# Kernel optimization log

Measured on AMD Instinct MI355X. Metric: run time of the kernel, lower is better.

Reference implementation:

```python
import jax, jax.numpy as jnp
import numpy as np
from jax import lax

B, T, D_IN = 16, 512, 128
H_ENC, D_LAT, H_CTX, H_PRED = 512, 256, 512, 512
K_STEPS, TEMP = 12, 0.1


def setup_inputs() -> dict:
    ks = jax.random.split(jax.random.key(0), 8)
    def w(i, fi, fo):
        return jax.random.normal(ks[i], (fi, fo), jnp.float32) * (1.0 / float(np.sqrt(fi)))
    return {
        "x": jax.random.normal(ks[0], (B, T, D_IN), jnp.float32),
        "enc_w1": w(1, D_IN, H_ENC), "enc_b1": jnp.zeros((H_ENC,), jnp.float32),
        "enc_w2": w(2, H_ENC, H_ENC), "enc_b2": jnp.zeros((H_ENC,), jnp.float32),
        "enc_w3": w(3, H_ENC, D_LAT), "enc_b3": jnp.zeros((D_LAT,), jnp.float32),
        "gru_wi": w(4, D_LAT, 3 * H_CTX), "gru_bi": jnp.zeros((3 * H_CTX,), jnp.float32),
        "gru_wh": w(5, H_CTX, 3 * H_CTX), "gru_bhn": jnp.zeros((H_CTX,), jnp.float32),
        "pred_w1": w(6, H_CTX, H_PRED), "pred_b1": jnp.zeros((H_PRED,), jnp.float32),
        "pred_w2": w(7, H_PRED, D_LAT), "pred_b2": jnp.zeros((D_LAT,), jnp.float32),
    }


def _gru(z, gru_wi, gru_bi, gru_wh, gru_bhn):
    # flax GRUCell: r=sig(Wir x + bir + Whr h); u=sig(Wiz x + biz + Whz h);
    Bsz = z.shape[0]
    H = gru_wh.shape[0]
    xi = z @ gru_wi + gru_bi          # [B, T, 3H] precomputed input projections
    xi = jnp.swapaxes(xi, 0, 1)       # [T, B, 3H]

    def step(h, x_t):
        hp = h @ gru_wh               # [B, 3H]
        xr, xu, xn = jnp.split(x_t, 3, axis=-1)
        hr, hu, hn = jnp.split(hp, 3, axis=-1)
        r = jax.nn.sigmoid(xr + hr)
        u = jax.nn.sigmoid(xu + hu)
        n = jnp.tanh(xn + r * (hn + gru_bhn))
        h_new = (1.0 - u) * n + u * h
        return h_new, h_new

    h0 = jnp.zeros((Bsz, H), z.dtype)
    _, outs = lax.scan(step, h0, xi)  # [T, B, H]
    return jnp.swapaxes(outs, 0, 1)   # [B, T, H]


def reference(x, enc_w1, enc_b1, enc_w2, enc_b2, enc_w3, enc_b3,
              gru_wi, gru_bi, gru_wh, gru_bhn,
              pred_w1, pred_b1, pred_w2, pred_b2):
    # Encoder MLP
    h = jax.nn.relu(x @ enc_w1 + enc_b1)
    h = jax.nn.relu(h @ enc_w2 + enc_b2)
    z = h @ enc_w3 + enc_b3                         # [B, T, D_LAT]
    # GRU context network
    c = _gru(z, gru_wi, gru_bi, gru_wh, gru_bhn)    # [B, T, H_CTX]
    # InfoNCE loss (prediction net is identical across k, so hoist it)
    c_t = c[:, :-K_STEPS, :].reshape(-1, c.shape[-1])   # [N, H_CTX], N=B*(T-K)
    p = jax.nn.relu(c_t @ pred_w1 + pred_b1) @ pred_w2 + pred_b2
    p = p / jnp.linalg.norm(p, axis=1, keepdims=True)   # [N, D_LAT]
    total = jnp.zeros((), z.dtype)
    for k in range(1, K_STEPS + 1):
        zt = z[:, k:T - K_STEPS + k, :].reshape(-1, z.shape[-1])
        zt = zt / jnp.linalg.norm(zt, axis=1, keepdims=True)
        sim = (p @ zt.T) / TEMP                         # [N, N]
        # -mean(diag(log_softmax)) = -mean(diag(sim) - logsumexp(sim, axis=1))
        total = total + (-jnp.mean(jnp.diagonal(sim) - jax.nn.logsumexp(sim, axis=1)))
    loss = total / K_STEPS
    return z, c, loss
```

## Files before the change

### kernel.cpp

```cpp
#include <hip/hip_runtime.h>
#include <cstdint>
#include <cstddef>

typedef unsigned short u16;
typedef unsigned int   u32;
typedef unsigned long long u64;
typedef __attribute__((ext_vector_type(8))) short bf16x8;
typedef __attribute__((ext_vector_type(4))) float f32x4;
typedef __attribute__((ext_vector_type(4))) unsigned int u32x4;

typedef __attribute__((address_space(1))) const unsigned int as1c_uint;
typedef __attribute__((address_space(3))) unsigned int as3_uint;

__device__ __forceinline__ void async16(const void* g, void* l) {
  __builtin_amdgcn_global_load_lds((as1c_uint*)g, (as3_uint*)l, 16, 0, 0);
}
__device__ __forceinline__ float bf2f(u16 u) {
  return __uint_as_float(((u32)u) << 16);
}
__device__ __forceinline__ u16 f2bf(float x) {
  u32 u = __float_as_uint(x);
  u32 r = u + 0x7FFFu + ((u >> 16) & 1u);
  return (u16)(r >> 16);
}

__device__ __forceinline__ u32 ld_u32_ic(const void* p) {
  u32 v;
  asm volatile("global_load_dword %0, %1, off sc0 sc1\n\ts_waitcnt vmcnt(0)"
               : "=v"(v) : "v"(p) : "memory");
  return v;
}
__device__ __forceinline__ void st_u32_ic(void* p, u32 v) {
  asm volatile("global_store_dword %0, %1, off sc0 sc1" :: "v"(p), "v"(v) : "memory");
}
__device__ __forceinline__ void ld_h64_ic(const void* p, u32x4& a, u32x4& b,
                                          u32x4& c, u32x4& d) {
  asm volatile(
      "global_load_dwordx4 %0, %4, off sc0 sc1\n\t"
      "global_load_dwordx4 %1, %4, off offset:16 sc0 sc1\n\t"
      "global_load_dwordx4 %2, %4, off offset:32 sc0 sc1\n\t"
      "global_load_dwordx4 %3, %4, off offset:48 sc0 sc1\n\t"
      "s_waitcnt vmcnt(0)"
      : "=&v"(a), "=&v"(b), "=&v"(c), "=&v"(d) : "v"(p) : "memory");
}

__global__ void cvt_k(const float4* __restrict__ in, ushort4* __restrict__ out) {
  int i = blockIdx.x * 256 + threadIdx.x;
  float4 v = in[i];
  ushort4 o;
  o.x = f2bf(v.x); o.y = f2bf(v.y); o.z = f2bf(v.z); o.w = f2bf(v.w);
  out[i] = o;
}

__global__ void tr_k(const float* __restrict__ in, u16* __restrict__ out, int K, int N) {
  __shared__ u16 t[32][33];
  int bn = blockIdx.x * 32, bk = blockIdx.y * 32;
  int x = threadIdx.x, y = threadIdx.y;
#pragma unroll
  for (int i = 0; i < 32; i += 8)
    t[y + i][x] = f2bf(in[(size_t)(bk + y + i) * N + bn + x]);
  __syncthreads();
#pragma unroll
  for (int i = 0; i < 32; i += 8)
    out[(size_t)(bn + y + i) * K + bk + x] = t[x][y + i];
}

__global__ __launch_bounds__(256) void gemm_k(
    const u16* __restrict__ A, const u16* __restrict__ Bt,
    const float* __restrict__ bias, u16* __restrict__ Cbf, float* __restrict__ Cf,
    int N, int K, int act) {
  __shared__ __align__(16) u16 As[128 * 32];
  __shared__ __align__(16) u16 Bs[128 * 32];
  int tid = threadIdx.x;
  int lane = tid & 63, w = tid >> 6;
  int wm = w >> 1, wn = w & 1;
  int mm = lane & 15, kh = lane >> 4;
  int m0 = blockIdx.y * 128, n0 = blockIdx.x * 128;

  f32x4 zero = {0.f, 0.f, 0.f, 0.f};
  f32x4 acc[4][4];
#pragma unroll
  for (int i = 0; i < 4; ++i)
#pragma unroll
    for (int j = 0; j < 4; ++j) acc[i][j] = zero;

  for (int kt = 0; kt < K; kt += 32) {
#pragma unroll
    for (int it = 0; it < 2; ++it) {
      int q = tid + it * 256;
      int row = q >> 2, kc = (q & 3) * 8;
      async16(A  + (size_t)(m0 + row) * K + kt + kc, &As[q * 8]);
      async16(Bt + (size_t)(n0 + row) * K + kt + kc, &Bs[q * 8]);
    }
    __syncthreads();
    bf16x8 av[4], bv[4];
#pragma unroll
    for (int i = 0; i < 4; ++i) {
      av[i] = *(const bf16x8*)&As[(wm * 64 + i * 16 + mm) * 32 + kh * 8];
      bv[i] = *(const bf16x8*)&Bs[(wn * 64 + i * 16 + mm) * 32 + kh * 8];
    }
#pragma unroll
    for (int im = 0; im < 4; ++im)
#pragma unroll
      for (int in = 0; in < 4; ++in)
        acc[im][in] = __builtin_amdgcn_mfma_f32_16x16x32_bf16(av[im], bv[in], acc[im][in], 0, 0, 0);
    __syncthreads();
  }

#pragma unroll
  for (int im = 0; im < 4; ++im)
#pragma unroll
    for (int in = 0; in < 4; ++in)
#pragma unroll
      for (int r = 0; r < 4; ++r) {
        int gm = m0 + wm * 64 + im * 16 + kh * 4 + r;
        int gn = n0 + wn * 64 + in * 16 + mm;
        float v = acc[im][in][r] + bias[gn];
        if (act) v = fmaxf(v, 0.f);
        size_t off = (size_t)gm * N + gn;
        if (Cbf) Cbf[off] = f2bf(v);
        if (Cf)  Cf[off]  = v;
      }
}

__global__ __launch_bounds__(256) void norm_k(const u16* __restrict__ in,
                                              u16* __restrict__ out, int pack) {
  int row = blockIdx.x * 4 + (threadIdx.x >> 6);
  int lane = threadIdx.x & 63;
  ushort4 v = ((const ushort4*)(in + (size_t)row * 256))[lane];
  float a = bf2f(v.x), b = bf2f(v.y), c = bf2f(v.z), d = bf2f(v.w);
  float s = a * a + b * b + c * c + d * d;
#pragma unroll
  for (int o = 32; o; o >>= 1) s += __shfl_xor(s, o);
  float rn = rsqrtf(s);
  int orow = row;
  if (pack) {
    int bb = row >> 9, tt = row & 511;
    if (tt >= 500) return;
    orow = bb * 500 + tt;
  }
  ushort4 o4;
  o4.x = f2bf(a * rn); o4.y = f2bf(b * rn);
  o4.z = f2bf(c * rn); o4.w = f2bf(d * rn);
  *(ushort4*)(out + (size_t)orow * 256 + lane * 4) = o4;
}

#define HS 520

__global__ __launch_bounds__(512, 1) void gru_k(
    const u16* __restrict__ xi, const float* __restrict__ WH,
    const float* __restrict__ BHN, float* __restrict__ cf,
    u16* __restrict__ cbf, u16* hbuf, u32* flags) {
  __shared__ __align__(16) u16 hs[16 * HS];
  __shared__ float xis[2 * 1536];
  __shared__ float gts[1536];
  __shared__ float hnf[512];

  int tid = threadIdx.x;
  int role = blockIdx.x;
  int c0 = role * 32;

  int lane = tid & 63, w = tid >> 6;
  int mm = lane & 15, kh = lane >> 4;

  bf16x8 wf[16];
  if (w < 6) {
    int gcol = (w >> 1) * 512 + c0 + (w & 1) * 16 + mm;
    int kb = kh * 8;
#pragma unroll
    for (int kk = 0; kk < 16; ++kk) {
      bf16x8 tf;
#pragma unroll
      for (int j = 0; j < 8; ++j)
        tf[j] = (short)f2bf(WH[(size_t)(kk * 32 + kb + j) * 1536 + gcol]);
      wf[kk] = tf;
    }
  }
  int cr = tid >> 4, cj = (tid & 15) * 2;
  float bhn0 = 0.f, bhn1 = 0.f;
  if (w < 4) { bhn0 = BHN[c0 + cj]; bhn1 = BHN[c0 + cj + 1]; }

  int tt = tid - 384;
  size_t xoff[12];
  u16 xpre[12];
  if (w >= 6) {
#pragma unroll
    for (int j = 0; j < 12; ++j) {
      int v = j * 128 + tt;
      int b = v / 96, q = v - b * 96;
      int gcol = (q >> 5) * 512 + c0 + (q & 31);
      xoff[j] = (size_t)b * 512 * 1536 + gcol;
      xis[v] = bf2f(xi[xoff[j]]);
    }
#pragma unroll
    for (int j = 0; j < 12; ++j) xpre[j] = xi[xoff[j] + 1536];
  }

  for (int t = 0; t < 512; ++t) {
    if (w < 4) {
      if (t == 0) {
        for (int i = tid; i < 16 * HS; i += 256) hs[i] = 0;
      } else {
        int iter = 0;
        const u32* fl = &flags[tid & 15];
        while (ld_u32_ic(fl) < (u32)t) { if (++iter > (1 << 22)) break; }
        const u16* hb = hbuf + (size_t)(t & 1) * 8192 + (tid >> 4) * 512 + (tid & 15) * 32;
        u32x4 a, b, c, d;
        ld_h64_ic(hb, a, b, c, d);
        u32x4* dst = (u32x4*)&hs[(tid >> 4) * HS + (tid & 15) * 32];
        dst[0] = a; dst[1] = b; dst[2] = c; dst[3] = d;
      }
    } else if (w >= 6) {
      if (t > 0) {
        int v = tt * 4;
        int b = v >> 5, col = v & 31;
        size_t co = ((size_t)b * 512 + (t - 1)) * 512 + c0 + col;
        float4 o;
        o.x = hnf[v]; o.y = hnf[v + 1]; o.z = hnf[v + 2]; o.w = hnf[v + 3];
        *(float4*)&cf[co] = o;
        uint2 pk;
        pk.x = (u32)f2bf(o.x) | ((u32)f2bf(o.y) << 16);
        pk.y = (u32)f2bf(o.z) | ((u32)f2bf(o.w) << 16);
        *(uint2*)&cbf[co] = pk;
      }
      if (t < 511) {
        float* xd = &xis[((t + 1) & 1) * 1536];
#pragma unroll
        for (int j = 0; j < 12; ++j) xd[j * 128 + tt] = bf2f(xpre[j]);
      }
      if (t < 510) {
        const u16* xs = xi + (size_t)(t + 2) * 1536;
#pragma unroll
        for (int j = 0; j < 12; ++j) xpre[j] = xs[xoff[j]];
      }
    }
    __syncthreads();

    if (w < 6) {
      f32x4 acc = {0.f, 0.f, 0.f, 0.f};
#pragma unroll
      for (int kk = 0; kk < 16; ++kk) {
        bf16x8 a = *(const bf16x8*)&hs[mm * HS + kk * 32 + kh * 8];
        acc = __builtin_amdgcn_mfma_f32_16x16x32_bf16(a, wf[kk], acc, 0, 0, 0);
      }
      int gc = (w >> 1) * 32 + (w & 1) * 16 + mm;
#pragma unroll
      for (int r = 0; r < 4; ++r) gts[(kh * 4 + r) * 96 + gc] = acc[r];
    }
    __syncthreads();

    if (w < 4) {
      const float* xc = &xis[(t & 1) * 1536] + cr * 96;
      const float* gr_ = &gts[cr * 96];
      float hp0 = bf2f(hs[cr * HS + c0 + cj]);
      float hp1 = bf2f(hs[cr * HS + c0 + cj + 1]);
      float r0 = 1.f / (1.f + __expf(-(xc[cj] + gr_[cj])));
      float u0 = 1.f / (1.f + __expf(-(xc[32 + cj] + gr_[32 + cj])));
      float nx0 = xc[64 + cj] + r0 * (gr_[64 + cj] + bhn0);
      float n0 = 1.f - 2.f / (__expf(2.f * nx0) + 1.f);
      float h0 = (1.f - u0) * n0 + u0 * hp0;
      float r1 = 1.f / (1.f + __expf(-(xc[cj + 1] + gr_[cj + 1])));
      float u1 = 1.f / (1.f + __expf(-(xc[33 + cj] + gr_[33 + cj])));
      float nx1 = xc[65 + cj] + r1 * (gr_[65 + cj] + bhn1);
      float n1 = 1.f - 2.f / (__expf(2.f * nx1) + 1.f);
      float h1v = (1.f - u1) * n1 + u1 * hp1;
      hnf[cr * 32 + cj] = h0;
      hnf[cr * 32 + cj + 1] = h1v;
      u32 pk = (u32)f2bf(h0) | ((u32)f2bf(h1v) << 16);
      st_u32_ic(hbuf + (size_t)((t + 1) & 1) * 8192 + cr * 512 + c0 + cj, pk);
      asm volatile("s_waitcnt vmcnt(0)" ::: "memory");
    }
    __syncthreads();
    if (tid == 0) st_u32_ic(&flags[role], (u32)(t + 1));
  }

  if (w >= 6) {
    int v = tt * 4;
    int b = v >> 5, col = v & 31;
    size_t co = ((size_t)b * 512 + 511) * 512 + c0 + col;
    float4 o;
    o.x = hnf[v]; o.y = hnf[v + 1]; o.z = hnf[v + 2]; o.w = hnf[v + 3];
    *(float4*)&cf[co] = o;
    uint2 pk;
    pk.x = (u32)f2bf(o.x) | ((u32)f2bf(o.y) << 16);
    pk.y = (u32)f2bf(o.z) | ((u32)f2bf(o.w) << 16);
    *(uint2*)&cbf[co] = pk;
  }
}

__global__ __launch_bounds__(256) void sgemm_k(
    const u16* __restrict__ P, const u16* __restrict__ Z,
    float* __restrict__ g, float* __restrict__ diag) {
  __shared__ __align__(16) u16 Ap[128 * 256];
  __shared__ __align__(16) u16 Bs[128 * 32];
  __shared__ float gacc[128 * 128];
  int tid = threadIdx.x;
  int lane = tid & 63, w = tid >> 6;
  int wm = w >> 1, wn = w & 1;
  int mm = lane & 15, kh = lane >> 4;
  int r0 = blockIdx.y * 128, t0 = blockIdx.x * 128;

#pragma unroll
  for (int it = 0; it < 16; ++it) {
    int q = tid + it * 256;
    int row = q >> 5, kc = (q & 31) * 8;
    async16(P + (size_t)(r0 + row) * 256 + kc, &Ap[q * 8]);
  }
  for (int i = tid; i < 128 * 128; i += 256) gacc[i] = 0.f;
  __syncthreads();

  f32x4 zero = {0.f, 0.f, 0.f, 0.f};
  for (int b = 0; b < 16; ++b) {
    int n0 = b * 512 + t0;
    f32x4 acc[4][4];
#pragma unroll
    for (int i = 0; i < 4; ++i)
#pragma unroll
      for (int j = 0; j < 4; ++j) acc[i][j] = zero;

    for (int kk = 0; kk < 8; ++kk) {
#pragma unroll
      for (int it = 0; it < 2; ++it) {
        int q = tid + it * 256;
        int row = q >> 2, kc = (q & 3) * 8;
        async16(Z + (size_t)(n0 + row) * 256 + kk * 32 + kc, &Bs[q * 8]);
      }
      __syncthreads();
      bf16x8 av[4], bv[4];
#pragma unroll
      for (int i = 0; i < 4; ++i) {
        av[i] = *(const bf16x8*)&Ap[(wm * 64 + i * 16 + mm) * 256 + kk * 32 + kh * 8];
        bv[i] = *(const bf16x8*)&Bs[(wn * 64 + i * 16 + mm) * 32 + kh * 8];
      }
#pragma unroll
      for (int im = 0; im < 4; ++im)
#pragma unroll
        for (int in = 0; in < 4; ++in)
          acc[im][in] = __builtin_amdgcn_mfma_f32_16x16x32_bf16(av[im], bv[in], acc[im][in], 0, 0, 0);
      __syncthreads();
    }
#pragma unroll
    for (int im = 0; im < 4; ++im)
#pragma unroll
      for (int in = 0; in < 4; ++in)
#pragma unroll
        for (int r = 0; r < 4; ++r) {
          int row = wm * 64 + im * 16 + kh * 4 + r;
          int col = wn * 64 + in * 16 + mm;
          float s10 = acc[im][in][r] * 10.f;
          gacc[row * 128 + col] += __expf(s10 - 10.f);
          int ig = r0 + row;
          if (ig < 8000) {
            int bi = ig / 500;
            if (bi == b) {
              int ti = ig - bi * 500;
              int dt = t0 + col - ti;
              if (dt >= 1 && dt <= 12) diag[(size_t)ig * 12 + dt - 1] = s10;
            }
          }
        }
  }
  __syncthreads();
  for (int i = tid; i < 128 * 128; i += 256) {
    int row = i >> 7, col = i & 127;
    g[(size_t)(r0 + row) * 512 + t0 + col] = gacc[i];
  }
}

__global__ __launch_bounds__(256) void win_k(const float* __restrict__ g,
                                             const float* __restrict__ diag,
                                             float* __restrict__ acc) {
  __shared__ float lo[4][16], hi[4][16];
  int w = threadIdx.x >> 6, lane = threadIdx.x & 63;
  int row = blockIdx.x * 4 + w;
  const float* gr = g + (size_t)row * 512;
  float4 a = ((const float4*)gr)[lane * 2];
  float4 b = ((const float4*)gr)[lane * 2 + 1];
  float s = a.x + a.y + a.z + a.w + b.x + b.y + b.z + b.w;
#pragma unroll
  for (int o = 32; o; o >>= 1) s += __shfl_xor(s, o);
  if (lane == 0) { lo[w][0]=a.x; lo[w][1]=a.y; lo[w][2]=a.z; lo[w][3]=a.w;
                   lo[w][4]=b.x; lo[w][5]=b.y; lo[w][6]=b.z; lo[w][7]=b.w; }
  if (lane == 1) { lo[w][8]=a.x; lo[w][9]=a.y; lo[w][10]=a.z; lo[w][11]=a.w; }
  if (lane == 62){ hi[w][0]=b.x; hi[w][1]=b.y; hi[w][2]=b.z; hi[w][3]=b.w; }
  if (lane == 63){ hi[w][4]=a.x; hi[w][5]=a.y; hi[w][6]=a.z; hi[w][7]=a.w;
                   hi[w][8]=b.x; hi[w][9]=b.y; hi[w][10]=b.z; hi[w][11]=b.w; }
  __syncthreads();
  float term = 0.f;
  if (lane < 12) {
    int k = lane + 1;
    float pre = 0.f, suf = 0.f;
#pragma unroll
    for (int j = 0; j < 12; ++j) {
      if (j < k) pre += lo[w][j];
      if (j >= k) suf += hi[w][j];
    }
    float W = s - pre - suf;
    term = diag[(size_t)row * 12 + lane] - __logf(W) - 10.f;
  }
#pragma unroll
  for (int o = 32; o; o >>= 1) term += __shfl_xor(term, o);
  if (lane == 0) atomicAdd(acc, term);
}

__global__ void fin_k(const float* acc, float* lout) {
  lout[0] = -acc[0] * (1.f / 96000.f);
}

extern "C" void kernel_launch(void* const* d_in, const int* in_sizes, int n_in,
                              void* d_out, int out_size, void* d_ws, size_t ws_size,
                              hipStream_t stream) {
  (void)in_sizes; (void)n_in; (void)out_size; (void)ws_size;
  const float* x    = (const float*)d_in[0];
  const float* ew1  = (const float*)d_in[1];
  const float* eb1  = (const float*)d_in[2];
  const float* ew2  = (const float*)d_in[3];
  const float* eb2  = (const float*)d_in[4];
  const float* ew3  = (const float*)d_in[5];
  const float* eb3  = (const float*)d_in[6];
  const float* gwi  = (const float*)d_in[7];
  const float* gbi  = (const float*)d_in[8];
  const float* gwh  = (const float*)d_in[9];
  const float* gbhn = (const float*)d_in[10];
  const float* pw1  = (const float*)d_in[11];
  const float* pb1  = (const float*)d_in[12];
  const float* pw2  = (const float*)d_in[13];
  const float* pb2  = (const float*)d_in[14];

  char* W = (char*)d_ws;
  u32*   flags = (u32*)(W + 64);
  float* lacc = (float*)(W + 2048);
  u16*   w1T  = (u16*)(W + 4096);
  u16*   w2T  = (u16*)(W + 135168);
  u16*   w3T  = (u16*)(W + 659456);
  u16*   wiT  = (u16*)(W + 921600);
  u16*   p1T  = (u16*)(W + 1708032);
  u16*   p2T  = (u16*)(W + 2232320);
  u16*   hbuf = (u16*)(W + 2494464);
  float* diag = (float*)(W + 2527232);
  u16*   zhat = (u16*)(W + 2911232);
  u16*   zbf  = (u16*)(W + 7105536);
  u16*   cbf  = (u16*)(W + 7105536);
  u16*   ppk  = (u16*)(W + 7105536);
  u16*   xi   = (u16*)(W + 15494144);
  u16*   xbf  = (u16*)(W + 15494144);
  u16*   h1   = (u16*)(W + 17591296);
  u16*   h2   = (u16*)(W + 25979904);
  float* g    = (float*)(W + 15494144);

  float* zf    = (float*)d_out;
  float* cf    = zf + 2097152;
  float* lout  = zf + 6291456;

  hipMemsetAsync(d_ws, 0, 4096, stream);

  cvt_k<<<1024, 256, 0, stream>>>((const float4*)x, (ushort4*)xbf);

  dim3 tb(32, 8);
  tr_k<<<dim3(16, 4),  tb, 0, stream>>>(ew1, w1T, 128, 512);
  tr_k<<<dim3(16, 16), tb, 0, stream>>>(ew2, w2T, 512, 512);
  tr_k<<<dim3(8, 16),  tb, 0, stream>>>(ew3, w3T, 512, 256);
  tr_k<<<dim3(48, 8),  tb, 0, stream>>>(gwi, wiT, 256, 1536);
  tr_k<<<dim3(16, 16), tb, 0, stream>>>(pw1, p1T, 512, 512);
  tr_k<<<dim3(8, 16),  tb, 0, stream>>>(pw2, p2T, 512, 256);

  gemm_k<<<dim3(4, 64),  256, 0, stream>>>(xbf,  w1T, eb1, h1,  nullptr, 512, 128, 1);
  gemm_k<<<dim3(4, 64),  256, 0, stream>>>(h1,   w2T, eb2, h2,  nullptr, 512, 512, 1);
  gemm_k<<<dim3(2, 64),  256, 0, stream>>>(h2,   w3T, eb3, zbf, zf,      256, 512, 0);
  norm_k<<<2048, 256, 0, stream>>>(zbf, zhat, 0);
  gemm_k<<<dim3(12, 64), 256, 0, stream>>>(zbf,  wiT, gbi, xi,  nullptr, 1536, 256, 0);
  gru_k<<<16, 512, 0, stream>>>(xi, gwh, gbhn, cf, cbf, hbuf, flags);
  gemm_k<<<dim3(4, 64),  256, 0, stream>>>(cbf,  p1T, pb1, h1,  nullptr, 512, 512, 1);
  gemm_k<<<dim3(2, 64),  256, 0, stream>>>(h1,   p2T, pb2, h2,  nullptr, 256, 512, 0);
  norm_k<<<2048, 256, 0, stream>>>(h2, ppk, 1);
  sgemm_k<<<dim3(4, 63), 256, 0, stream>>>(ppk, zhat, g, diag);
  win_k<<<2000, 256, 0, stream>>>(g, diag, lacc);
  fin_k<<<1, 1, 0, stream>>>(lacc, lout);
}
```

Measured before the change: 1.910 ms.

## Embed step tags in GRU hidden-state exchange instead of separate flag handshake

The cross-block GRU synchronisation no longer uses a per-block flag that is written after a barrier and then polled before the hidden state is read. Each 4-byte bf16 pair is now stored together with its timestep tag as an 8-byte unit, and consumers poll the data itself until every tag matches. This removes the store-wait, flag store and separate flag-polling round trip from the serial 512-step critical path. The cost is that the exchange buffer doubles in size, so each poll reads twice as many bytes, and the buffer must be zeroed before launch.

```diff
diff --git a/kernel.cpp b/kernel.cpp
--- a/kernel.cpp
+++ b/kernel.cpp
@@ -8,6 +8,7 @@
 typedef __attribute__((ext_vector_type(8))) short bf16x8;
 typedef __attribute__((ext_vector_type(4))) float f32x4;
 typedef __attribute__((ext_vector_type(4))) unsigned int u32x4;
+typedef __attribute__((ext_vector_type(2))) unsigned int u32x2;
 
 typedef __attribute__((address_space(1))) const unsigned int as1c_uint;
 typedef __attribute__((address_space(3))) unsigned int as3_uint;
@@ -24,24 +25,25 @@
   return (u16)(r >> 16);
 }
 
-__device__ __forceinline__ u32 ld_u32_ic(const void* p) {
-  u32 v;
-  asm volatile("global_load_dword %0, %1, off sc0 sc1\n\ts_waitcnt vmcnt(0)"
-               : "=v"(v) : "v"(p) : "memory");
-  return v;
-}
-__device__ __forceinline__ void st_u32_ic(void* p, u32 v) {
-  asm volatile("global_store_dword %0, %1, off sc0 sc1" :: "v"(p), "v"(v) : "memory");
-}
-__device__ __forceinline__ void ld_h64_ic(const void* p, u32x4& a, u32x4& b,
-                                          u32x4& c, u32x4& d) {
+__device__ __forceinline__ void st_unit_ic(void* p, u32x2 v) {
+  asm volatile("global_store_dwordx2 %0, %1, off sc0 sc1" :: "v"(p), "v"(v) : "memory");
+}
+__device__ __forceinline__ void ld_units_ic(const void* p,
+    u32x4& a, u32x4& b, u32x4& c, u32x4& d,
+    u32x4& e, u32x4& f, u32x4& g2, u32x4& h) {
   asm volatile(
-      "global_load_dwordx4 %0, %4, off sc0 sc1\n\t"
-      "global_load_dwordx4 %1, %4, off offset:16 sc0 sc1\n\t"
-      "global_load_dwordx4 %2, %4, off offset:32 sc0 sc1\n\t"
-      "global_load_dwordx4 %3, %4, off offset:48 sc0 sc1\n\t"
+      "global_load_dwordx4 %0, %8, off sc0 sc1\n\t"
+      "global_load_dwordx4 %1, %8, off offset:16 sc0 sc1\n\t"
+      "global_load_dwordx4 %2, %8, off offset:32 sc0 sc1\n\t"
+      "global_load_dwordx4 %3, %8, off offset:48 sc0 sc1\n\t"
+      "global_load_dwordx4 %4, %8, off offset:64 sc0 sc1\n\t"
+      "global_load_dwordx4 %5, %8, off offset:80 sc0 sc1\n\t"
+      "global_load_dwordx4 %6, %8, off offset:96 sc0 sc1\n\t"
+      "global_load_dwordx4 %7, %8, off offset:112 sc0 sc1\n\t"
       "s_waitcnt vmcnt(0)"
-      : "=&v"(a), "=&v"(b), "=&v"(c), "=&v"(d) : "v"(p) : "memory");
+      : "=&v"(a), "=&v"(b), "=&v"(c), "=&v"(d),
+        "=&v"(e), "=&v"(f), "=&v"(g2), "=&v"(h)
+      : "v"(p) : "memory");
 }
 
 __global__ void cvt_k(const float4* __restrict__ in, ushort4* __restrict__ out) {
@@ -150,7 +152,7 @@
 __global__ __launch_bounds__(512, 1) void gru_k(
     const u16* __restrict__ xi, const float* __restrict__ WH,
     const float* __restrict__ BHN, float* __restrict__ cf,
-    u16* __restrict__ cbf, u16* hbuf, u32* flags) {
+    u16* __restrict__ cbf, u16* hbuf) {
   __shared__ __align__(16) u16 hs[16 * HS];
   __shared__ float xis[2 * 1536];
   __shared__ float gts[1536];
@@ -159,6 +161,7 @@
   int tid = threadIdx.x;
   int role = blockIdx.x;
   int c0 = role * 32;
+  char* hb8 = (char*)hbuf;
 
   int lane = tid & 63, w = tid >> 6;
   int mm = lane & 15, kh = lane >> 4;
@@ -201,14 +204,26 @@
       if (t == 0) {
         for (int i = tid; i < 16 * HS; i += 256) hs[i] = 0;
       } else {
+        const char* hb = hb8 + ((size_t)(t & 1)) * 32768 +
+                         ((size_t)((tid >> 4) * 256 + (tid & 15) * 16)) * 8;
+        u32 tv = (u32)t;
+        u32x4 a, b, c, d, e, f, g2, h;
         int iter = 0;
-        const u32* fl = &flags[tid & 15];
-        while (ld_u32_ic(fl) < (u32)t) { if (++iter > (1 << 22)) break; }
-        const u16* hb = hbuf + (size_t)(t & 1) * 8192 + (tid >> 4) * 512 + (tid & 15) * 32;
-        u32x4 a, b, c, d;
-        ld_h64_ic(hb, a, b, c, d);
+        for (;;) {
+          ld_units_ic(hb, a, b, c, d, e, f, g2, h);
+          bool ok = (a.y == tv) & (a.w == tv) & (b.y == tv) & (b.w == tv) &
+                    (c.y == tv) & (c.w == tv) & (d.y == tv) & (d.w == tv) &
+                    (e.y == tv) & (e.w == tv) & (f.y == tv) & (f.w == tv) &
+                    (g2.y == tv) & (g2.w == tv) & (h.y == tv) & (h.w == tv);
+          if (ok || ++iter > (1 << 22)) break;
+        }
         u32x4* dst = (u32x4*)&hs[(tid >> 4) * HS + (tid & 15) * 32];
-        dst[0] = a; dst[1] = b; dst[2] = c; dst[3] = d;
+        u32x4 o0, o1, o2, o3;
+        o0.x = a.x;  o0.y = a.z;  o0.z = b.x;  o0.w = b.z;
+        o1.x = c.x;  o1.y = c.z;  o1.z = d.x;  o1.w = d.z;
+        o2.x = e.x;  o2.y = e.z;  o2.z = f.x;  o2.w = f.z;
+        o3.x = g2.x; o3.y = g2.z; o3.z = h.x;  o3.w = h.z;
+        dst[0] = o0; dst[1] = o1; dst[2] = o2; dst[3] = o3;
       }
     } else if (w >= 6) {
       if (t > 0) {
@@ -266,12 +281,13 @@
       float h1v = (1.f - u1) * n1 + u1 * hp1;
       hnf[cr * 32 + cj] = h0;
       hnf[cr * 32 + cj + 1] = h1v;
-      u32 pk = (u32)f2bf(h0) | ((u32)f2bf(h1v) << 16);
-      st_u32_ic(hbuf + (size_t)((t + 1) & 1) * 8192 + cr * 512 + c0 + cj, pk);
-      asm volatile("s_waitcnt vmcnt(0)" ::: "memory");
+      u32x2 un;
+      un.x = (u32)f2bf(h0) | ((u32)f2bf(h1v) << 16);
+      un.y = (u32)(t + 1);
+      st_unit_ic(hb8 + ((size_t)((t + 1) & 1)) * 32768 +
+                 ((size_t)(cr * 256 + role * 16 + (tid & 15))) * 8, un);
     }
     __syncthreads();
-    if (tid == 0) st_u32_ic(&flags[role], (u32)(t + 1));
   }
 
   if (w >= 6) {
@@ -428,7 +444,6 @@
   const float* pb2  = (const float*)d_in[14];
 
   char* W = (char*)d_ws;
-  u32*   flags = (u32*)(W + 64);
   float* lacc = (float*)(W + 2048);
   u16*   w1T  = (u16*)(W + 4096);
   u16*   w2T  = (u16*)(W + 135168);
@@ -437,22 +452,23 @@
   u16*   p1T  = (u16*)(W + 1708032);
   u16*   p2T  = (u16*)(W + 2232320);
   u16*   hbuf = (u16*)(W + 2494464);
-  float* diag = (float*)(W + 2527232);
-  u16*   zhat = (u16*)(W + 2911232);
-  u16*   zbf  = (u16*)(W + 7105536);
-  u16*   cbf  = (u16*)(W + 7105536);
-  u16*   ppk  = (u16*)(W + 7105536);
-  u16*   xi   = (u16*)(W + 15494144);
-  u16*   xbf  = (u16*)(W + 15494144);
-  u16*   h1   = (u16*)(W + 17591296);
-  u16*   h2   = (u16*)(W + 25979904);
-  float* g    = (float*)(W + 15494144);
+  float* diag = (float*)(W + 2560000);
+  u16*   zhat = (u16*)(W + 2944000);
+  u16*   zbf  = (u16*)(W + 7138304);
+  u16*   cbf  = (u16*)(W + 7138304);
+  u16*   ppk  = (u16*)(W + 7138304);
+  u16*   xi   = (u16*)(W + 15526912);
+  u16*   xbf  = (u16*)(W + 15526912);
+  u16*   h1   = (u16*)(W + 17624064);
+  u16*   h2   = (u16*)(W + 26012672);
+  float* g    = (float*)(W + 15526912);
 
   float* zf    = (float*)d_out;
   float* cf    = zf + 2097152;
   float* lout  = zf + 6291456;
 
   hipMemsetAsync(d_ws, 0, 4096, stream);
+  hipMemsetAsync((void*)hbuf, 0, 65536, stream);
 
   cvt_k<<<1024, 256, 0, stream>>>((const float4*)x, (ushort4*)xbf);
 
@@ -469,7 +485,7 @@
   gemm_k<<<dim3(2, 64),  256, 0, stream>>>(h2,   w3T, eb3, zbf, zf,      256, 512, 0);
   norm_k<<<2048, 256, 0, stream>>>(zbf, zhat, 0);
   gemm_k<<<dim3(12, 64), 256, 0, stream>>>(zbf,  wiT, gbi, xi,  nullptr, 1536, 256, 0);
-  gru_k<<<16, 512, 0, stream>>>(xi, gwh, gbhn, cf, cbf, hbuf, flags);
+  gru_k<<<16, 512, 0, stream>>>(xi, gwh, gbhn, cf, cbf, hbuf);
   gemm_k<<<dim3(4, 64),  256, 0, stream>>>(cbf,  p1T, pb1, h1,  nullptr, 512, 512, 1);
   gemm_k<<<dim3(2, 64),  256, 0, stream>>>(h1,   p2T, pb2, h2,  nullptr, 256, 512, 0);
   norm_k<<<2048, 256, 0, stream>>>(h2, ppk, 1);
```

Result: slower. 2.029 ms (+6.3%).
